# Performance work log

Hardware: AMD Instinct MI355X
Metric: run time of the kernel (lower is better)

## Reference

```python
import jax, jax.numpy as jnp
import numpy as np

# dims (see shape_source)
B, NC, DIM_IN = 4, 4095, 64      # batch, cells, invariant state dim (n-6)
D, H, L, K = 128, 4, 2, 6        # d_model, heads, layers, num_neighbors
DH = D // H                      # dim_head = 32
HR, NRBF = 16, 16                # radial hidden dim (d_model//8), rbf basis
RBF_MAX, RBF_W = 4.0, 0.25


def _ln(x, s, b):
    m = x.mean(-1, keepdims=True)
    v = x.var(-1, keepdims=True)
    return (x - m) / jnp.sqrt(v + 1e-5) * s + b


def setup_inputs() -> dict:
    key = jax.random.key(0)
    ks = jax.random.split(key, 32)
    def nrm(k, shape, scale):
        return jax.random.normal(k, shape, jnp.float32) * scale
    p = {}
    p['X'] = nrm(ks[0], (B, NC, 6 + DIM_IN), 1.0)
    p['W_embed'] = nrm(ks[1], (DIM_IN, D), DIM_IN ** -0.5)
    p['b_embed'] = jnp.zeros((D,), jnp.float32)
    p['Wq'] = nrm(ks[2], (L, D, D), D ** -0.5)
    p['Wk'] = nrm(ks[3], (L, D, D), D ** -0.5)
    p['Wv'] = nrm(ks[4], (L, D, D), D ** -0.5)
    p['Wvv'] = nrm(ks[5], (L, D, D), D ** -0.5)
    p['rw1'] = nrm(ks[6], (L, NRBF, HR), NRBF ** -0.5)
    p['rb1'] = jnp.zeros((L, HR), jnp.float32)
    p['rw2'] = nrm(ks[7], (L, HR, 2 * D), HR ** -0.5)
    p['rb2'] = jnp.zeros((L, 2 * D), jnp.float32)
    p['Wo'] = nrm(ks[8], (L, D, D), D ** -0.5)
    p['Wov'] = nrm(ks[9], (L, D, D), D ** -0.5)
    p['ff_w1'] = nrm(ks[10], (L, D, 2 * D), D ** -0.5)
    p['ff_b1'] = jnp.zeros((L, 2 * D), jnp.float32)
    p['ff_w2'] = nrm(ks[11], (L, 2 * D, D), (2 * D) ** -0.5)
    p['ff_b2'] = jnp.zeros((L, D), jnp.float32)
    p['gate_w'] = nrm(ks[12], (L, D, D), D ** -0.5)
    p['gate_b'] = jnp.zeros((L, D), jnp.float32)
    p['ln1_s'] = jnp.ones((L, D), jnp.float32)
    p['ln1_b'] = jnp.zeros((L, D), jnp.float32)
    p['ln2_s'] = jnp.ones((L, D), jnp.float32)
    p['ln2_b'] = jnp.zeros((L, D), jnp.float32)
    p['W_state'] = nrm(ks[13], (D, DIM_IN), D ** -0.5)
    p['b_state'] = jnp.zeros((DIM_IN,), jnp.float32)
    p['W_force'] = nrm(ks[14], (D, 1), D ** -0.5)
    p['b_force'] = jnp.zeros((1,), jnp.float32)
    return p


def _forward(X, W_embed, b_embed, Wq, Wk, Wv, Wvv, rw1, rb1, rw2, rb2, Wo, Wov,
             ff_w1, ff_b1, ff_w2, ff_b2, gate_w, gate_b,
             ln1_s, ln1_b, ln2_s, ln2_b, W_state, b_state, W_force, b_force):
    N = NC + 1  # one extra zero node prepended, as in the torch wrapper
    pos = jnp.concatenate([jnp.zeros((B, 1, 3), X.dtype), X[:, :, 0:3]], axis=1)       # [B,N,3]
    feats = jnp.concatenate([jnp.zeros((B, 1, DIM_IN), X.dtype), X[:, :, 6:]], axis=1)  # [B,N,dim_in]

    # k-nearest-neighbor graph (indices are non-differentiable constants)
    d2 = jnp.sum((pos[:, :, None, :] - pos[:, None, :, :]) ** 2, axis=-1)  # [B,N,N]
    d2 = d2 + jnp.eye(N, dtype=X.dtype) * 1e9                               # exclude self
    _, idx = jax.lax.top_k(-d2, K)                                           # [B,N,K]

    gat = lambda a: jax.vmap(lambda ai, ii: ai[ii])(a, idx)  # [B,N,...] -> [B,N,K,...]

    rel = gat(pos) - pos[:, :, None, :]                      # [B,N,K,3]
    dist = jnp.sqrt(jnp.sum(rel ** 2, axis=-1) + 1e-8)       # [B,N,K]
    u = rel / dist[..., None]                                # unit vectors (degree-1 SH)
    centers = jnp.linspace(0.0, RBF_MAX, NRBF).astype(X.dtype)
    rbf = jnp.exp(-((dist[..., None] - centers) / RBF_W) ** 2)  # [B,N,K,NRBF]

    x0 = feats @ W_embed + b_embed                           # type-0 (invariant) feats
    x1 = jnp.zeros((B, N, D, 3), X.dtype)                    # type-1 (vector) feats

    for l in range(L):
        h = _ln(x0, ln1_s[l], ln1_b[l])
        q = (h @ Wq[l]).reshape(B, N, H, DH)
        kj = gat(h @ Wk[l]).reshape(B, N, K, H, DH)
        vj = gat(h @ Wv[l])                                   # [B,N,K,D]
        # radial MLP on distances -> invariant edge weights
        rad = jax.nn.silu(rbf @ rw1[l] + rb1[l]) @ rw2[l] + rb2[l]  # [B,N,K,2D]
        rg, rv = rad[..., :D], rad[..., D:]
        bias = rg.reshape(B, N, K, H, DH).mean(-1)            # [B,N,K,H]
        logits = jnp.einsum('bnhd,bnkhd->bnhk', q, kj) / np.float32(np.sqrt(DH))
        logits = logits + bias.transpose(0, 1, 3, 2)
        attn = jax.nn.softmax(logits, axis=-1)                # over K neighbors
        # degree-0 messages
        m0 = (vj * jax.nn.silu(rv)).reshape(B, N, K, H, DH)
        out0 = jnp.einsum('bnhk,bnkhd->bnhd', attn, m0).reshape(B, N, D)
        x0 = x0 + out0 @ Wo[l]
        # degree-1 messages: channel-mixed neighbor vectors + radial-weighted unit dirs
        x1j = gat(x1)                                          # [B,N,K,D,3]
        m1 = jnp.einsum('bnkdc,de->bnkec', x1j, Wvv[l]) + rv[..., None] * u[:, :, :, None, :]
        m1 = m1.reshape(B, N, K, H, DH, 3)
        out1 = jnp.einsum('bnhk,bnkhdc->bnhdc', attn, m1).reshape(B, N, D, 3)
        x1 = x1 + jnp.einsum('bndc,de->bnec', out1, Wov[l])
        # feed-forward on invariants + invariant gating of vectors (equivariant)
        h2 = _ln(x0, ln2_s[l], ln2_b[l])
        x0 = x0 + jax.nn.silu(h2 @ ff_w1[l] + ff_b1[l]) @ ff_w2[l] + ff_b2[l]
        x1 = x1 * jax.nn.sigmoid(h2 @ gate_w[l] + gate_b[l])[..., None]

    y0 = x0[:, 1:]                                            # drop extra node
    y1 = jnp.swapaxes(x1[:, 1:], -1, -2)                      # [B,NC,3,D]
    state_update = y0 @ W_state + b_state                     # [B,NC,dim_in]
    forces = (y1 @ W_force + b_force)[..., 0]                 # [B,NC,3]
    forces = forces - forces.mean(axis=1, keepdims=True)      # remove net force
    return state_update, forces


def reference(X, W_embed, b_embed, Wq, Wk, Wv, Wvv, rw1, rb1, rw2, rb2, Wo, Wov,
              ff_w1, ff_b1, ff_w2, ff_b2, gate_w, gate_b,
              ln1_s, ln1_b, ln2_s, ln2_b, W_state, b_state, W_force, b_force):
    return _forward(X, W_embed, b_embed, Wq, Wk, Wv, Wvv, rw1, rb1, rw2, rb2, Wo, Wov,
                    ff_w1, ff_b1, ff_w2, ff_b2, gate_w, gate_b,
                    ln1_s, ln1_b, ln2_s, ln2_b, W_state, b_state, W_force, b_force)
```

## Files before the change

kernel.cpp:

```cpp
#include <hip/hip_runtime.h>
#include <cstdint>
#include <cstddef>

namespace {

constexpr int B_ = 4, NC_ = 4095, N_ = 4096, DIN_ = 64, D_ = 128, K_ = 6;
constexpr int XROW_ = 6 + DIN_;
constexpr int ROWS_ = B_ * N_;
constexpr int KNQ = 2;
constexpr int KCAP = 32;

typedef unsigned short u16;
typedef unsigned int u32;
typedef unsigned long long u64;
typedef __attribute__((ext_vector_type(8))) short short8;
typedef __attribute__((ext_vector_type(4))) float f32x4;

__device__ __forceinline__ float sigm(float x) { return 1.f / (1.f + expf(-x)); }
__device__ __forceinline__ float silu(float x) { return x / (1.f + expf(-x)); }
__device__ __forceinline__ u16 f2bf(float x) {
    u32 u = __float_as_uint(x);
    u += 0x7FFFu + ((u >> 16) & 1u);
    return (u16)(u >> 16);
}
__device__ __forceinline__ float bf2f(u16 x) {
    return __uint_as_float(((u32)x) << 16);
}

__device__ __forceinline__ void prep_body(const float* __restrict__ X, float4* __restrict__ pos4,
                                          u16* __restrict__ featsb, int g)
{
    if (g >= ROWS_ * 64) return;
    int c = g & 63, row = g >> 6;
    int b = row >> 12, n = row & (N_ - 1);
    const float* xr = X + (size_t)(b * NC_ + n - 1) * XROW_;
    featsb[g] = (n > 0) ? f2bf(xr[6 + c]) : (u16)0;
    if (c == 0) {
        float4 p = {0.f, 0.f, 0.f, 0.f};
        if (n > 0) { p.x = xr[0]; p.y = xr[1]; p.z = xr[2]; }
        pos4[row] = p;
    }
}

__device__ __forceinline__ void prepw_body(int l, int g,
    const float* Wq, const float* Wk, const float* Wv, const float* gw,
    const float* fw1, const float* gb_, const float* fb1, const float* Wvv,
    const float* Wov, const float* Wo_, const float* fw2, const float* rw2,
    const float* rb2, const float* W_embed, const float* rw1,
    u16* WqkvT, u16* Wc2T, u16* WvvT, u16* WovT, u16* WoT, u16* fw2T, u16* WembT,
    float* bias2, float* rwg, float* rw1T, float* rw2vT)
{
    const float* Wq_l = Wq + l * 16384;  const float* Wk_l = Wk + l * 16384;
    const float* Wv_l = Wv + l * 16384;  const float* gw_l = gw + l * 16384;
    const float* fw1_l = fw1 + l * 32768; const float* gb_l = gb_ + l * 128;
    const float* fb1_l = fb1 + l * 256;  const float* Wvv_l = Wvv + l * 16384;
    const float* Wov_l = Wov + l * 16384; const float* Wo_ll = Wo_ + l * 16384;
    const float* fw2_l = fw2 + l * 32768; const float* rw2_l = rw2 + l * 4096;
    const float* rb2_l = rb2 + l * 256;  const float* rw1_l = rw1 + l * 256;

    if (g < 49152) {
        int n = g >> 7, k = g & 127;
        const float* src = (n < 128) ? Wq_l : ((n < 256) ? Wk_l : Wv_l);
        WqkvT[l * 49152 + g] = f2bf(src[k * 128 + (n & 127)]); return;
    }
    g -= 49152;
    if (g < 49152) {
        int n = g >> 7, k = g & 127;
        Wc2T[l * 49152 + g] = f2bf((n < 128) ? gw_l[k * 128 + n] : fw1_l[k * 256 + (n - 128)]); return;
    }
    g -= 49152;
    if (g < 16384) { int n = g >> 7, k = g & 127; WvvT[l * 16384 + g] = f2bf(Wvv_l[k * 128 + n]); return; }
    g -= 16384;
    if (g < 16384) { int n = g >> 7, k = g & 127; WovT[l * 16384 + g] = f2bf(Wov_l[k * 128 + n]); return; }
    g -= 16384;
    if (g < 16384) { int n = g >> 7, k = g & 127; WoT[l * 16384 + g] = f2bf(Wo_ll[k * 128 + n]); return; }
    g -= 16384;
    if (g < 32768) { int n = g >> 8, k = g & 255; fw2T[l * 32768 + g] = f2bf(fw2_l[k * 128 + n]); return; }
    g -= 32768;
    if (g < 384) { bias2[l * 384 + g] = (g < 128) ? gb_l[g] : fb1_l[g - 128]; return; }
    g -= 384;
    if (g < 64) {
        int hh = g >> 2, h = g & 3;
        float a = 0.f;
        #pragma unroll
        for (int dh = 0; dh < 32; ++dh) a += rw2_l[hh * 256 + h * 32 + dh];
        rwg[l * 128 + g] = a * (1.f / 32.f); return;
    }
    g -= 64;
    if (g < 4) {
        float a = 0.f;
        #pragma unroll
        for (int dh = 0; dh < 32; ++dh) a += rb2_l[g * 32 + dh];
        rwg[l * 128 + 64 + g] = a * (1.f / 32.f); return;
    }
    g -= 4;
    if (g < 256) {
        int hh = g >> 4, rr = g & 15;
        rw1T[l * 256 + hh * 16 + rr] = rw1_l[rr * 16 + hh]; return;
    }
    g -= 256;
    if (g < 2048) {
        int t = g >> 4, hh = g & 15;
        rw2vT[l * 2048 + t * 16 + hh] = rw2_l[hh * 256 + 128 + t]; return;
    }
    g -= 2048;
    if (g < 8192 && l == 0) {
        int n = g >> 6, k = g & 63;
        WembT[g] = f2bf(W_embed[k * 128 + n]);
    }
}

__global__ void k_prepall(const float* __restrict__ X, float4* __restrict__ pos4,
                          u16* __restrict__ featsb,
                          const float* Wq, const float* Wk, const float* Wv, const float* gw,
                          const float* fw1, const float* gb_, const float* fb1, const float* Wvv,
                          const float* Wov, const float* Wo_, const float* fw2, const float* rw2,
                          const float* rb2, const float* W_embed, const float* rw1,
                          u16* WqkvT, u16* Wc2T, u16* WvvT, u16* WovT, u16* WoT, u16* fw2T,
                          u16* WembT, float* bias2, float* rwg, float* rw1T, float* rw2vT)
{
    int id = blockIdx.x;
    if (id < 4096) {
        prep_body(X, pos4, featsb, id * 256 + threadIdx.x);
    } else {
        int id2 = id - 4096;
        int l = id2 / 747, gx = id2 % 747;
        prepw_body(l, gx * 256 + threadIdx.x, Wq, Wk, Wv, gw, fw1, gb_, fb1, Wvv, Wov, Wo_,
                   fw2, rw2, rb2, W_embed, rw1, WqkvT, Wc2T, WvvT, WovT, WoT, fw2T, WembT,
                   bias2, rwg, rw1T, rw2vT);
    }
}

__device__ __forceinline__ u64 shflxor64(u64 v, int mask)
{
    int lo = __shfl_xor((int)(u32)(v & 0xffffffffull), mask, 64);
    int hi = __shfl_xor((int)(u32)(v >> 32), mask, 64);
    return ((u64)(u32)hi << 32) | (u32)lo;
}

__device__ __forceinline__ float kth7min(float v)
{
    const float BIG = 3.4e38f;
    float kth = BIG;
    #pragma unroll
    for (int r = 0; r < 7; ++r) {
        float m = v;
        #pragma unroll
        for (int off = 1; off < 64; off <<= 1) m = fminf(m, __shfl_xor(m, off, 64));
        kth = m;
        if (v == m) v = BIG;
    }
    return kth;
}

__device__ __forceinline__ void geom_write(const float4* __restrict__ pb, int q, int j,
                                           size_t e, float* __restrict__ uv,
                                           float* __restrict__ rbfv)
{
    float4 pj = pb[j], pn = pb[q];
    float rx = pj.x - pn.x, ry = pj.y - pn.y, rz = pj.z - pn.z;
    float dist = sqrtf(rx * rx + ry * ry + rz * rz + 1e-8f);
    float inv = 1.f / dist;
    uv[e * 3 + 0] = rx * inv; uv[e * 3 + 1] = ry * inv; uv[e * 3 + 2] = rz * inv;
    #pragma unroll
    for (int r = 0; r < 16; ++r) {
        float t = (dist - (4.0f / 15.0f) * r) * 4.0f;
        rbfv[e * 16 + r] = expf(-t * t);
    }
}

__global__ __launch_bounds__(256) void k_knn(const float4* __restrict__ pos4,
                                             int* __restrict__ idxv,
                                             float* __restrict__ uv,
                                             float* __restrict__ rbfv)
{
    __shared__ u64 sHits[4][KNQ][KCAP];
    __shared__ int sCnt[4][KNQ];
    const int w = threadIdx.x >> 6, lane = threadIdx.x & 63;
    const int wave = (blockIdx.x << 2) | w;
    const int b = wave >> 11;
    const int i0 = (wave & 2047) << 1;
    const float4* pb = pos4 + (size_t)b * N_;
    const float BIG = 3.4e38f;

    if (lane < KNQ) sCnt[w][lane] = 0;
    __syncthreads();

    float4 qv[KNQ];
    #pragma unroll
    for (int qq = 0; qq < KNQ; ++qq) qv[qq] = pb[i0 + qq];

    float dmin[KNQ];
    #pragma unroll
    for (int qq = 0; qq < KNQ; ++qq) dmin[qq] = BIG;
    #pragma unroll 4
    for (int it = 0; it < 64; ++it) {
        int j = lane + (it << 6);
        float4 p = pb[j];
        #pragma unroll
        for (int qq = 0; qq < KNQ; ++qq) {
            float dx = p.x - qv[qq].x, dy = p.y - qv[qq].y, dz = p.z - qv[qq].z;
            float dd = dx * dx + dy * dy + dz * dz;
            dmin[qq] = fminf(dmin[qq], dd);
        }
    }
    float T[KNQ];
    #pragma unroll
    for (int qq = 0; qq < KNQ; ++qq) T[qq] = kth7min(dmin[qq]) * 1.000002f;

    #pragma unroll 4
    for (int it = 0; it < 64; ++it) {
        int j = lane + (it << 6);
        float4 p = pb[j];
        #pragma unroll
        for (int qq = 0; qq < KNQ; ++qq) {
            float dx = p.x - qv[qq].x, dy = p.y - qv[qq].y, dz = p.z - qv[qq].z;
            float dd = dx * dx + dy * dy + dz * dz;
            if (dd <= T[qq] && j != i0 + qq) {
                int slot = atomicAdd(&sCnt[w][qq], 1);
                if (slot < KCAP)
                    sHits[w][qq][slot] = ((u64)__float_as_uint(dd) << 32) | (u32)j;
            }
        }
    }
    __syncthreads();

    const int g = lane >> 5, li = lane & 31;
    const int cnt = sCnt[w][g];
    const int q = i0 + g;
    u64 ent = (li < (cnt < KCAP ? cnt : KCAP)) ? sHits[w][g][li] : ~0ull;
    int myj = -1;
    #pragma unroll
    for (int k = 0; k < 6; ++k) {
        u64 m = ent;
        #pragma unroll
        for (int off = 1; off < 32; off <<= 1) {
            u64 o = shflxor64(m, off);
            if (o < m) m = o;
        }
        if (li == k) myj = (int)(u32)(m & 0xffffffffull);
        if (ent == m) ent = ~0ull;
    }
    if (cnt <= KCAP && li < 6) {
        size_t e = (size_t)(b * N_ + q) * 6 + li;
        idxv[e] = myj;
        geom_write(pb, q, myj, e, uv, rbfv);
    }

    u64 ovf = __ballot(li == 0 && cnt > KCAP);
    while (ovf) {
        int gl = __ffsll(ovf) - 1; ovf &= ovf - 1;
        int qq = gl >> 5;
        int qx = i0 + qq;
        float4 qp = pb[qx];
        float Tq = T[0];
        #pragma unroll
        for (int z = 1; z < KNQ; ++z) if (z == qq) Tq = T[z];
        float e0 = BIG, e1 = BIG, e2 = BIG, e3 = BIG, e4 = BIG, e5 = BIG;
        int j0 = 0, j1 = 0, j2 = 0, j3 = 0, j4 = 0, j5 = 0;
        for (int it = 0; it < 64; ++it) {
            int j = lane + (it << 6);
            float4 p = pb[j];
            float dx = p.x - qp.x, dy = p.y - qp.y, dz = p.z - qp.z;
            float dd = dx * dx + dy * dy + dz * dz;
            if (dd <= Tq && j != qx && dd < e5) {
                e5 = dd; j5 = j;
                float td; int tj;
                if (e5 < e4) { td = e4; e4 = e5; e5 = td; tj = j4; j4 = j5; j5 = tj; }
                if (e4 < e3) { td = e3; e3 = e4; e4 = td; tj = j3; j3 = j4; j4 = tj; }
                if (e3 < e2) { td = e2; e2 = e3; e3 = td; tj = j2; j2 = j3; j3 = tj; }
                if (e2 < e1) { td = e1; e1 = e2; e2 = td; tj = j1; j1 = j2; j2 = tj; }
                if (e1 < e0) { td = e0; e0 = e1; e1 = td; tj = j0; j0 = j1; j1 = tj; }
            }
        }
        u64 a0 = ((u64)__float_as_uint(e0) << 32) | (u32)j0;
        u64 a1 = ((u64)__float_as_uint(e1) << 32) | (u32)j1;
        u64 a2 = ((u64)__float_as_uint(e2) << 32) | (u32)j2;
        u64 a3 = ((u64)__float_as_uint(e3) << 32) | (u32)j3;
        u64 a4 = ((u64)__float_as_uint(e4) << 32) | (u32)j4;
        u64 a5 = ((u64)__float_as_uint(e5) << 32) | (u32)j5;
        int fj = -1;
        #pragma unroll
        for (int k = 0; k < 6; ++k) {
            u64 m = a0;
            #pragma unroll
            for (int off = 1; off < 64; off <<= 1) {
                u64 o = shflxor64(m, off);
                if (o < m) m = o;
            }
            if (a0 == m) { a0 = a1; a1 = a2; a2 = a3; a3 = a4; a4 = a5; a5 = ~0ull; }
            if (lane == k) fj = (int)(u32)(m & 0xffffffffull);
        }
        if (lane < 6) {
            size_t e = (size_t)(b * N_ + qx) * 6 + lane;
            idxv[e] = fj;
            geom_write(pb, qx, fj, e, uv, rbfv);
        }
    }
}

template<int KD, int BM, int EPI, bool LN, bool X1ACC>
__device__ __forceinline__ void mgemm_body(
    const u16* __restrict__ A, const u16* __restrict__ WT,
    const float* __restrict__ bias, const float* __restrict__ aux,
    float* __restrict__ C, u16* __restrict__ Cb, int ldc,
    const float* __restrict__ lns, const float* __restrict__ lnb,
    u16* __restrict__ lnout,
    int bx, int by, u16* sA, u16* sB, float* sLNraw)
{
    constexpr int MI = BM / 16;
    float (*sLN)[4][2] = (float(*)[4][2])sLNraw;
    const int tid = threadIdx.x;
    const int lane = tid & 63, wn = tid >> 6;
    const int m0 = bx * BM, n0 = by * 128;
    f32x4 acc[MI][2] = {};

    const bool aload = (BM == 64) || (tid < BM * 4);
    const int arow = tid >> 2, agk = tid & 3;
    const int c0 = tid * 2, c1 = tid * 2 + 1;
    const int brow0 = c0 >> 2, bgk0 = c0 & 3;
    const int brow1 = c1 >> 2, bgk1 = c1 & 3;

    uint4 ra = {}, rb0v, rb1v;
    if (aload) ra = *(const uint4*)&A[(size_t)(m0 + arow) * KD + agk * 8];
    rb0v = *(const uint4*)&WT[(size_t)(n0 + brow0) * KD + bgk0 * 8];
    rb1v = *(const uint4*)&WT[(size_t)(n0 + brow1) * KD + bgk1 * 8];

    #pragma unroll
    for (int k0 = 0; k0 < KD; k0 += 32) {
        if (aload) *(uint4*)&sA[arow * 40 + agk * 8] = ra;
        *(uint4*)&sB[brow0 * 40 + bgk0 * 8] = rb0v;
        *(uint4*)&sB[brow1 * 40 + bgk1 * 8] = rb1v;
        __syncthreads();
        if (k0 + 32 < KD) {
            if (aload) ra = *(const uint4*)&A[(size_t)(m0 + arow) * KD + k0 + 32 + agk * 8];
            rb0v = *(const uint4*)&WT[(size_t)(n0 + brow0) * KD + k0 + 32 + bgk0 * 8];
            rb1v = *(const uint4*)&WT[(size_t)(n0 + brow1) * KD + k0 + 32 + bgk1 * 8];
        }
        const int gk = lane >> 4, lr = lane & 15;
        short8 af[MI], bfr[2];
        #pragma unroll
        for (int i = 0; i < MI; ++i)
            af[i] = *(const short8*)&sA[(i * 16 + lr) * 40 + gk * 8];
        #pragma unroll
        for (int i = 0; i < 2; ++i)
            bfr[i] = *(const short8*)&sB[(wn * 32 + i * 16 + lr) * 40 + gk * 8];
        #pragma unroll
        for (int mi = 0; mi < MI; ++mi)
            #pragma unroll
            for (int ni = 0; ni < 2; ++ni)
                acc[mi][ni] = __builtin_amdgcn_mfma_f32_16x16x32_bf16(af[mi], bfr[ni], acc[mi][ni], 0, 0, 0);
        __syncthreads();
    }

    const int lg = lane >> 4;
    const int lc = lane & 15;
    if (LN) {
        float s1[MI][4], s2[MI][4];
        #pragma unroll
        for (int mi = 0; mi < MI; ++mi) {
            int rbase = m0 + mi * 16 + lg * 4;
            #pragma unroll
            for (int ee = 0; ee < 4; ++ee) { s1[mi][ee] = 0.f; s2[mi][ee] = 0.f; }
            #pragma unroll
            for (int ni = 0; ni < 2; ++ni) {
                int col = wn * 32 + ni * 16 + lc;
                float bc = bias ? bias[col] : 0.f;
                #pragma unroll
                for (int ee = 0; ee < 4; ++ee) {
                    float v = acc[mi][ni][ee] + bc;
                    if (EPI == 1) v += C[(size_t)(rbase + ee) * 128 + col];
                    acc[mi][ni][ee] = v;
                    s1[mi][ee] += v;
                    s2[mi][ee] += v * v;
                }
            }
        }
        #pragma unroll
        for (int mi = 0; mi < MI; ++mi)
            #pragma unroll
            for (int ee = 0; ee < 4; ++ee)
                #pragma unroll
                for (int off = 1; off < 16; off <<= 1) {
                    s1[mi][ee] += __shfl_xor(s1[mi][ee], off, 64);
                    s2[mi][ee] += __shfl_xor(s2[mi][ee], off, 64);
                }
        if (lc == 0) {
            #pragma unroll
            for (int mi = 0; mi < MI; ++mi)
                #pragma unroll
                for (int ee = 0; ee < 4; ++ee) {
                    int r = mi * 16 + lg * 4 + ee;
                    sLN[r][wn][0] = s1[mi][ee];
                    sLN[r][wn][1] = s2[mi][ee];
                }
        }
        __syncthreads();
        #pragma unroll
        for (int mi = 0; mi < MI; ++mi) {
            int rbase = m0 + mi * 16 + lg * 4;
            #pragma unroll
            for (int ee = 0; ee < 4; ++ee) {
                int r = mi * 16 + lg * 4 + ee;
                float sum = sLN[r][0][0] + sLN[r][1][0] + sLN[r][2][0] + sLN[r][3][0];
                float sq  = sLN[r][0][1] + sLN[r][1][1] + sLN[r][2][1] + sLN[r][3][1];
                float mean = sum * (1.f / 128.f);
                float var = sq * (1.f / 128.f) - mean * mean;
                float inv = 1.f / sqrtf(var + 1e-5f);
                #pragma unroll
                for (int ni = 0; ni < 2; ++ni) {
                    int col = wn * 32 + ni * 16 + lc;
                    float v = acc[mi][ni][ee];
                    size_t o = (size_t)(rbase + ee) * 128 + col;
                    C[o] = v;
                    lnout[o] = f2bf((v - mean) * inv * lns[col] + lnb[col]);
                }
            }
        }
        return;
    }

    #pragma unroll
    for (int mi = 0; mi < MI; ++mi) {
        int rbase = m0 + mi * 16 + lg * 4;
        #pragma unroll
        for (int ni = 0; ni < 2; ++ni) {
            int col = n0 + wn * 32 + ni * 16 + lc;
            if (EPI == 0) {
                float bc = bias ? bias[col] : 0.f;
                #pragma unroll
                for (int ee = 0; ee < 4; ++ee)
                    C[(size_t)(rbase + ee) * ldc + col] = acc[mi][ni][ee] + bc;
            } else if (EPI == 1) {
                float bc = bias ? bias[col] : 0.f;
                #pragma unroll
                for (int ee = 0; ee < 4; ++ee) {
                    size_t o = (size_t)(rbase + ee) * ldc + col;
                    C[o] += acc[mi][ni][ee] + bc;
                }
            } else if (EPI == 2) {
                float bc = bias[col];
                if (n0 == 0) {
                    #pragma unroll
                    for (int ee = 0; ee < 4; ++ee)
                        C[(size_t)(rbase + ee) * 128 + col] = sigm(acc[mi][ni][ee] + bc);
                } else {
                    int c2 = col - 128;
                    #pragma unroll
                    for (int ee = 0; ee < 4; ++ee)
                        Cb[(size_t)(rbase + ee) * 256 + c2] = f2bf(silu(acc[mi][ni][ee] + bc));
                }
            } else if (EPI == 4) {
                float bc = bias ? bias[col] : 0.f;
                #pragma unroll
                for (int ee = 0; ee < 4; ++ee)
                    Cb[(size_t)(rbase + ee) * ldc + col] = f2bf(acc[mi][ni][ee] + bc);
            } else {
                #pragma unroll
                for (int ee = 0; ee < 4; ++ee) {
                    int m = rbase + ee;
                    size_t o = (size_t)m * 128 + col;
                    float v = acc[mi][ni][ee];
                    if (X1ACC) v += C[o];
                    v *= aux[(size_t)(m / 3) * 128 + col];
                    C[o] = v;
                    Cb[o] = f2bf(v);
                }
            }
        }
    }
}

template<int KD, int BM, int EPI, bool LN, bool X1ACC>
__global__ __launch_bounds__(256) void k_mgemm(
    const u16* __restrict__ A, const u16* __restrict__ WT,
    const float* __restrict__ bias, const float* __restrict__ aux,
    float* __restrict__ C, u16* __restrict__ Cb, int ldc,
    const float* __restrict__ lns, const float* __restrict__ lnb,
    u16* __restrict__ lnout)
{
    __shared__ u16 sA[64 * 40];
    __shared__ u16 sB[128 * 40];
    __shared__ float sLN[64 * 4 * 2];
    mgemm_body<KD, BM, EPI, LN, X1ACC>(A, WT, bias, aux, C, Cb, ldc, lns, lnb, lnout,
                                       blockIdx.x, blockIdx.y, sA, sB, sLN);
}

template<int KD0, int BM0, int EPI0, bool LN0, bool XA0,
         int KD1, int BM1, int EPI1, bool LN1v, bool XA1>
__global__ __launch_bounds__(256) void k_mgemm_dual(
    const u16* A0, const u16* WT0, const float* b0, const float* aux0,
    float* C0, u16* Cb0, int ldc0, const float* lns0, const float* lnb0, u16* ln0,
    int nx0, int nxdiv0,
    const u16* A1, const u16* WT1, const float* b1, const float* aux1,
    float* C1, u16* Cb1, int ldc1, const float* lns1, const float* lnb1, u16* ln1)
{
    __shared__ u16 sA[64 * 40];
    __shared__ u16 sB[128 * 40];
    __shared__ float sLN[64 * 4 * 2];
    int id = blockIdx.x;
    if (id < nx0) {
        mgemm_body<KD0, BM0, EPI0, LN0, XA0>(A0, WT0, b0, aux0, C0, Cb0, ldc0, lns0, lnb0, ln0,
                                             id % nxdiv0, id / nxdiv0, sA, sB, sLN);
    } else {
        id -= nx0;
        mgemm_body<KD1, BM1, EPI1, LN1v, XA1>(A1, WT1, b1, aux1, C1, Cb1, ldc1, lns1, lnb1, ln1,
                                              id, 0, sA, sB, sLN);
    }
}

template<bool HASY1>
__global__ __launch_bounds__(256) void k_attn(
    const u16* __restrict__ qkvb, const int* __restrict__ idxv,
    const float* __restrict__ rbfv, const float* __restrict__ uv,
    const u16* __restrict__ y1b,
    const float* __restrict__ rw1T, const float* __restrict__ rb1,
    const float* __restrict__ rw2vT, const float* __restrict__ rwg,
    const float* __restrict__ rb2,
    u16* __restrict__ o0b, u16* __restrict__ o1b)
{
    const int wid = threadIdx.x >> 6, lane = threadIdx.x & 63;
    const int row = blockIdx.x * 4 + wid;
    const int b = row >> 12;
    const int ch0 = lane * 2;
    const int h = lane >> 4;

    __shared__ float sHid[4][6][16];
    __shared__ float sU[4][6][3];

    int jl = 0;
    if (lane < 6) jl = idxv[row * 6 + lane];
    int jj[6];
    #pragma unroll
    for (int k = 0; k < 6; ++k) jj[k] = __shfl(jl, k, 64);

    if (lane < 18) sU[wid][lane / 3][lane % 3] = uv[(size_t)row * 18 + lane];

    {
        int idx = lane;
        #pragma unroll
        for (int rep = 0; rep < 2; ++rep) {
            if (idx < 96) {
                int k = idx >> 4, hh = idx & 15;
                float a = rb1[hh];
                const float* rb = rbfv + (size_t)(row * 6 + k) * 16;
                const float* wr = rw1T + hh * 16;
                #pragma unroll
                for (int rr = 0; rr < 16; ++rr) a += rb[rr] * wr[rr];
                sHid[wid][k][hh] = silu(a);
            }
            idx += 64;
        }
    }
    __builtin_amdgcn_wave_barrier();
    __threadfence_block();
    __builtin_amdgcn_wave_barrier();

    u32 qp = *(const u32*)&qkvb[(size_t)row * 384 + ch0];
    float q0 = bf2f((u16)qp), q1 = bf2f((u16)(qp >> 16));

    float part[6];
    #pragma unroll
    for (int k = 0; k < 6; ++k) {
        u32 kp = *(const u32*)&qkvb[(size_t)(b * N_ + jj[k]) * 384 + 128 + ch0];
        part[k] = q0 * bf2f((u16)kp) + q1 * bf2f((u16)(kp >> 16));
    }
    #pragma unroll
    for (int off = 1; off < 16; off <<= 1)
        #pragma unroll
        for (int k = 0; k < 6; ++k)
            part[k] += __shfl_xor(part[k], off, 64);

    float lg[6];
    #pragma unroll
    for (int k = 0; k < 6; ++k) {
        float bias = rwg[64 + h];
        #pragma unroll
        for (int hh = 0; hh < 16; ++hh) bias += sHid[wid][k][hh] * rwg[hh * 4 + h];
        lg[k] = part[k] * 0.17677669529663687f + bias;
    }

    float mx = lg[0];
    #pragma unroll
    for (int k = 1; k < 6; ++k) mx = fmaxf(mx, lg[k]);
    float a[6], smv = 0.f;
    #pragma unroll
    for (int k = 0; k < 6; ++k) { a[k] = expf(lg[k] - mx); smv += a[k]; }
    float inv = 1.f / smv;
    #pragma unroll
    for (int k = 0; k < 6; ++k) a[k] *= inv;

    float rwc0[16], rwc1[16];
    {
        const float4* wp = (const float4*)(rw2vT + ch0 * 16);
        #pragma unroll
        for (int i = 0; i < 4; ++i) {
            float4 v0 = wp[i], v1 = wp[i + 4];
            rwc0[i * 4 + 0] = v0.x; rwc0[i * 4 + 1] = v0.y; rwc0[i * 4 + 2] = v0.z; rwc0[i * 4 + 3] = v0.w;
            rwc1[i * 4 + 0] = v1.x; rwc1[i * 4 + 1] = v1.y; rwc1[i * 4 + 2] = v1.z; rwc1[i * 4 + 3] = v1.w;
        }
    }
    float rb20 = rb2[128 + ch0], rb21 = rb2[128 + ch0 + 1];
    float rvk0[6], rvk1[6];
    #pragma unroll
    for (int k = 0; k < 6; ++k) {
        float a0 = rb20, a1 = rb21;
        #pragma unroll
        for (int hh = 0; hh < 16; ++hh) {
            float hv = sHid[wid][k][hh];
            a0 += hv * rwc0[hh];
            a1 += hv * rwc1[hh];
        }
        rvk0[k] = a0; rvk1[k] = a1;
    }

    float o00 = 0.f, o01 = 0.f;
    #pragma unroll
    for (int k = 0; k < 6; ++k) {
        u32 vp = *(const u32*)&qkvb[(size_t)(b * N_ + jj[k]) * 384 + 256 + ch0];
        o00 += a[k] * bf2f((u16)vp) * silu(rvk0[k]);
        o01 += a[k] * bf2f((u16)(vp >> 16)) * silu(rvk1[k]);
    }
    *(u32*)&o0b[(size_t)row * 128 + ch0] = (u32)f2bf(o00) | ((u32)f2bf(o01) << 16);

    #pragma unroll
    for (int c = 0; c < 3; ++c) {
        float s0 = 0.f, s1 = 0.f;
        #pragma unroll
        for (int k = 0; k < 6; ++k) {
            float b0 = 0.f, b1 = 0.f;
            if (HASY1) {
                u32 yp = *(const u32*)&y1b[((size_t)(b * N_ + jj[k]) * 3 + c) * 128 + ch0];
                b0 = bf2f((u16)yp); b1 = bf2f((u16)(yp >> 16));
            }
            float uk = sU[wid][k][c];
            s0 += a[k] * (b0 + rvk0[k] * uk);
            s1 += a[k] * (b1 + rvk1[k] * uk);
        }
        *(u32*)&o1b[((size_t)row * 3 + c) * 128 + ch0] = (u32)f2bf(s0) | ((u32)f2bf(s1) << 16);
    }
}

__global__ __launch_bounds__(256) void k_head(
    const float* __restrict__ x0, const float* __restrict__ W_state,
    const float* __restrict__ b_state, float* __restrict__ out,
    const float* __restrict__ x1, const float* __restrict__ W_force,
    const float* __restrict__ b_force, float* __restrict__ frc)
{
    __shared__ __align__(16) float As[32 * 132];
    __shared__ __align__(16) float Ws[32 * 68];
    const int tid = threadIdx.x;
    if (blockIdx.x < 128) {
        const int tx = tid & 15, ty = tid >> 4;
        const int m0 = blockIdx.x * 128, n0 = 0;
        float acc[8][4] = {};
        for (int k0 = 0; k0 < 128; k0 += 32) {
            __syncthreads();
            #pragma unroll
            for (int r = 0; r < 4; ++r) {
                int id = tid + r * 256;
                int row = id >> 3, kq = id & 7;
                float4 a4 = *(const float4*)&x0[(size_t)(m0 + row) * 128 + k0 + kq * 4];
                As[(kq * 4 + 0) * 132 + row] = a4.x;
                As[(kq * 4 + 1) * 132 + row] = a4.y;
                As[(kq * 4 + 2) * 132 + row] = a4.z;
                As[(kq * 4 + 3) * 132 + row] = a4.w;
            }
            #pragma unroll
            for (int r = 0; r < 2; ++r) {
                int id = tid + r * 256;
                int kr = id >> 4, cq = id & 15;
                *(float4*)&Ws[kr * 68 + cq * 4] =
                    *(const float4*)&W_state[(size_t)(k0 + kr) * 64 + n0 + cq * 4];
            }
            __syncthreads();
            #pragma unroll 8
            for (int k = 0; k < 32; ++k) {
                float4 aA = *(const float4*)&As[k * 132 + ty * 8];
                float4 aB = *(const float4*)&As[k * 132 + ty * 8 + 4];
                float4 w4 = *(const float4*)&Ws[k * 68 + tx * 4];
                float av[8] = {aA.x, aA.y, aA.z, aA.w, aB.x, aB.y, aB.z, aB.w};
                float wv[4] = {w4.x, w4.y, w4.z, w4.w};
                #pragma unroll
                for (int r = 0; r < 8; ++r)
                    #pragma unroll
                    for (int j = 0; j < 4; ++j)
                        acc[r][j] += av[r] * wv[j];
            }
        }
        float bv[4];
        #pragma unroll
        for (int j = 0; j < 4; ++j) bv[j] = b_state[n0 + tx * 4 + j];
        #pragma unroll
        for (int r = 0; r < 8; ++r) {
            int m = m0 + ty * 8 + r;
            int n = m & (N_ - 1), bb2 = m >> 12;
            if (n == 0) continue;
            float* dst = out + ((size_t)(bb2 * NC_ + n - 1)) * 64 + n0 + tx * 4;
            float4 res = {acc[r][0] + bv[0], acc[r][1] + bv[1], acc[r][2] + bv[2], acc[r][3] + bv[3]};
            *(float4*)dst = res;
        }
    } else {
        int g = (blockIdx.x - 128) * 256 + tid;
        if (g >= B_ * NC_ * 3) return;
        int c = g % 3, rr = g / 3;
        int b = rr / NC_, n = rr - b * NC_;
        const float* xr = x1 + (size_t)(b * N_ + n + 1) * 384 + c * 128;
        float a = b_force[0];
        for (int d = 0; d < 128; ++d) a += xr[d] * W_force[d];
        frc[g] = a;
    }
}

__global__ __launch_bounds__(256) void k_fsum(const float* __restrict__ frc, float* __restrict__ fsum)
{
    int b = blockIdx.x / 3, c = blockIdx.x % 3;
    __shared__ float red[256];
    float a = 0.f;
    for (int n = threadIdx.x; n < NC_; n += 256) a += frc[(b * NC_ + n) * 3 + c];
    red[threadIdx.x] = a; __syncthreads();
    for (int st = 128; st > 0; st >>= 1) { if (threadIdx.x < st) red[threadIdx.x] += red[threadIdx.x + st]; __syncthreads(); }
    if (threadIdx.x == 0) fsum[blockIdx.x] = red[0] / (float)NC_;
}

__global__ void k_force2(const float* __restrict__ frc, const float* __restrict__ fsum,
                         float* __restrict__ out)
{
    int g = blockIdx.x * 256 + threadIdx.x;
    if (g >= B_ * NC_ * 3) return;
    int c = g % 3;
    int b = g / (NC_ * 3);
    out[g] = frc[g] - fsum[b * 3 + c];
}

}

extern "C" void kernel_launch(void* const* d_in, const int* in_sizes, int n_in,
                              void* d_out, int out_size, void* d_ws, size_t ws_size,
                              hipStream_t stream)
{
    const float* X       = (const float*)d_in[0];
    const float* W_embed = (const float*)d_in[1];
    const float* b_embed = (const float*)d_in[2];
    const float* Wq      = (const float*)d_in[3];
    const float* Wk      = (const float*)d_in[4];
    const float* Wv      = (const float*)d_in[5];
    const float* Wvv     = (const float*)d_in[6];
    const float* rw1     = (const float*)d_in[7];
    const float* rb1     = (const float*)d_in[8];
    const float* rw2     = (const float*)d_in[9];
    const float* rb2     = (const float*)d_in[10];
    const float* Wo      = (const float*)d_in[11];
    const float* Wov     = (const float*)d_in[12];
    const float* ff_w1   = (const float*)d_in[13];
    const float* ff_b1   = (const float*)d_in[14];
    const float* ff_w2   = (const float*)d_in[15];
    const float* ff_b2   = (const float*)d_in[16];
    const float* gate_w  = (const float*)d_in[17];
    const float* gate_b  = (const float*)d_in[18];
    const float* ln1_s   = (const float*)d_in[19];
    const float* ln1_b   = (const float*)d_in[20];
    const float* ln2_s   = (const float*)d_in[21];
    const float* ln2_b   = (const float*)d_in[22];
    const float* W_state = (const float*)d_in[23];
    const float* b_state = (const float*)d_in[24];
    const float* W_force = (const float*)d_in[25];
    const float* b_force = (const float*)d_in[26];
    (void)in_sizes; (void)n_in; (void)out_size; (void)ws_size;

    float* out = (float*)d_out;
    float* w = (float*)d_ws;

    float4* pos4  = (float4*)w;
    int*    idxv  = (int*)(w + 65536);
    float*  uv    = w + 163840;
    float*  rbfv  = w + 458752;
    u16*    featsb= (u16*)(w + 2031616);
    float*  x0    = w + 2555904;
    u16*    hbb   = (u16*)(w + 4653056);
    u16*    qkvbb = (u16*)(w + 5701632);
    float*  gb    = w + 11993088;
    u16*    o0b   = (u16*)(w + 14090240);
    u16*    o1b   = (u16*)(w + 15138816);
    float*  x1    = w + 18284544;
    u16*    x1b   = (u16*)(w + 24576000);
    u16*    t1b   = (u16*)(w + 27721728);
    u16*    y1b   = t1b;
    u16*    WqkvT = (u16*)(w + 34013184);
    u16*    Wc2T  = (u16*)(w + 34062336);
    u16*    WvvT  = (u16*)(w + 34111488);
    u16*    WovT  = (u16*)(w + 34127872);
    u16*    WoT   = (u16*)(w + 34144256);
    u16*    fw2T  = (u16*)(w + 34160640);
    u16*    WembT = (u16*)(w + 34193408);
    float*  bias2 = w + 34197504;
    float*  rwg   = w + 34198272;
    float*  rw1T  = w + 34198528;
    float*  rw2vT = w + 34199040;
    float*  frc   = (float*)featsb;
    float*  fsum  = ((float*)featsb) + 49152;

    k_prepall<<<5590, 256, 0, stream>>>(X, pos4, featsb,
                                        Wq, Wk, Wv, gate_w, ff_w1, gate_b, ff_b1,
                                        Wvv, Wov, Wo, ff_w2, rw2, rb2, W_embed, rw1,
                                        WqkvT, Wc2T, WvvT, WovT, WoT, fw2T, WembT,
                                        bias2, rwg, rw1T, rw2vT);
    k_knn<<<ROWS_ / 8, 256, 0, stream>>>(pos4, idxv, uv, rbfv);
    k_mgemm<64, 32, 0, true, true><<<dim3(512, 1), 256, 0, stream>>>(
        featsb, WembT, b_embed, nullptr, x0, nullptr, 128, ln1_s, ln1_b, hbb);

    for (int l = 0; l < 2; ++l) {
        const float* rb1_l = rb1 + l * 16;
        const float* rb2_l = rb2 + l * 256;
        const float* fb2_l = ff_b2 + l * 128;

        if (l == 0)
            k_mgemm<128, 64, 4, false, true><<<dim3(256, 3), 256, 0, stream>>>(
                hbb, WqkvT, nullptr, nullptr, nullptr, qkvbb, 384, nullptr, nullptr, nullptr);
        else
            k_mgemm_dual<128, 64, 4, false, true, 128, 64, 4, false, true><<<1536, 256, 0, stream>>>(
                hbb, WqkvT + 49152, nullptr, nullptr, nullptr, qkvbb, 384, nullptr, nullptr, nullptr,
                768, 256,
                x1b, WvvT + 16384, nullptr, nullptr, nullptr, y1b, 128, nullptr, nullptr, nullptr);
        if (l == 0)
            k_attn<false><<<ROWS_ / 4, 256, 0, stream>>>(qkvbb, idxv, rbfv, uv, nullptr,
                rw1T + l * 256, rb1_l, rw2vT + l * 2048, rwg + l * 128, rb2_l, o0b, o1b);
        else
            k_attn<true><<<ROWS_ / 4, 256, 0, stream>>>(qkvbb, idxv, rbfv, uv, y1b,
                rw1T + l * 256, rb1_l, rw2vT + l * 2048, rwg + l * 128, rb2_l, o0b, o1b);
        k_mgemm<128, 32, 1, true, true><<<dim3(512, 1), 256, 0, stream>>>(
            o0b, WoT + l * 16384, nullptr, nullptr, x0, nullptr, 128,
            ln2_s + l * 128, ln2_b + l * 128, hbb);
        k_mgemm<128, 64, 2, false, true><<<dim3(256, 3), 256, 0, stream>>>(
            hbb, Wc2T + l * 49152, bias2 + l * 384, nullptr, gb, t1b, 128, nullptr, nullptr, nullptr);
        if (l == 0)
            k_mgemm_dual<128, 64, 3, false, false, 256, 32, 1, true, true><<<1280, 256, 0, stream>>>(
                o1b, WovT, nullptr, gb, x1, x1b, 128, nullptr, nullptr, nullptr,
                768, 768,
                t1b, fw2T, fb2_l, nullptr, x0, nullptr, 128, ln1_s + 128, ln1_b + 128, hbb);
        else
            k_mgemm_dual<128, 64, 3, false, true, 256, 32, 1, false, true><<<1280, 256, 0, stream>>>(
                o1b, WovT + 16384, nullptr, gb, x1, x1b, 128, nullptr, nullptr, nullptr,
                768, 768,
                t1b, fw2T + 32768, fb2_l, nullptr, x0, nullptr, 128, nullptr, nullptr, nullptr);
    }

    k_head<<<320, 256, 0, stream>>>(x0, W_state, b_state, out, x1, W_force, b_force, frc);
    k_fsum<<<12, 256, 0, stream>>>(frc, fsum);
    k_force2<<<(B_ * NC_ * 3 + 255) / 256, 256, 0, stream>>>(frc, fsum, out + (size_t)B_ * NC_ * DIN_);
}
```

Before: 286.0 us.

## Split KNN candidate scan across wave pairs with four queries per wave

Each wave now handles four queries over half of the candidate points, and the two waves of a pair merge their per-query thresholds through shared memory. Squared distance is computed as |p|^2+|q|^2-2p·q using a precomputed norm stored in pos4.w, and the exact difference form is recomputed only for accepted hits. The aim is more reuse of each loaded point and fewer FLOPs per pair. In exchange it adds a block barrier and a looser threshold margin, which may let in more hits and trigger the slow overflow path more often.

```diff
diff --git a/kernel.cpp b/kernel.cpp
--- a/kernel.cpp
+++ b/kernel.cpp
@@ -7,7 +7,6 @@
 constexpr int B_ = 4, NC_ = 4095, N_ = 4096, DIN_ = 64, D_ = 128, K_ = 6;
 constexpr int XROW_ = 6 + DIN_;
 constexpr int ROWS_ = B_ * N_;
-constexpr int KNQ = 2;
 constexpr int KCAP = 32;
 
 typedef unsigned short u16;
@@ -37,7 +36,7 @@
     featsb[g] = (n > 0) ? f2bf(xr[6 + c]) : (u16)0;
     if (c == 0) {
         float4 p = {0.f, 0.f, 0.f, 0.f};
-        if (n > 0) { p.x = xr[0]; p.y = xr[1]; p.z = xr[2]; }
+        if (n > 0) { p.x = xr[0]; p.y = xr[1]; p.z = xr[2]; p.w = p.x * p.x + p.y * p.y + p.z * p.z; }
         pos4[row] = p;
     }
 }
@@ -174,61 +173,75 @@
                                              float* __restrict__ uv,
                                              float* __restrict__ rbfv)
 {
-    __shared__ u64 sHits[4][KNQ][KCAP];
-    __shared__ int sCnt[4][KNQ];
+    __shared__ u64 sHits[8][KCAP];
+    __shared__ int sCnt[8];
+    __shared__ float sT[4][4];
     const int w = threadIdx.x >> 6, lane = threadIdx.x & 63;
-    const int wave = (blockIdx.x << 2) | w;
-    const int b = wave >> 11;
-    const int i0 = (wave & 2047) << 1;
+    const int pair = w >> 1, half = w & 1;
+    const int qglob0 = blockIdx.x * 8 + pair * 4;
+    const int b = qglob0 >> 12;
+    const int qwb0 = qglob0 & (N_ - 1);
     const float4* pb = pos4 + (size_t)b * N_;
+    const int jbase = half * 2048;
     const float BIG = 3.4e38f;
 
-    if (lane < KNQ) sCnt[w][lane] = 0;
+    if (threadIdx.x < 8) sCnt[threadIdx.x] = 0;
     __syncthreads();
 
-    float4 qv[KNQ];
-    #pragma unroll
-    for (int qq = 0; qq < KNQ; ++qq) qv[qq] = pb[i0 + qq];
-
-    float dmin[KNQ];
-    #pragma unroll
-    for (int qq = 0; qq < KNQ; ++qq) dmin[qq] = BIG;
+    float4 qv[4];
+    #pragma unroll
+    for (int qq = 0; qq < 4; ++qq) qv[qq] = pb[qwb0 + qq];
+
+    float dmin[4] = {BIG, BIG, BIG, BIG};
     #pragma unroll 4
-    for (int it = 0; it < 64; ++it) {
-        int j = lane + (it << 6);
+    for (int it = 0; it < 32; ++it) {
+        int j = jbase + lane + (it << 6);
         float4 p = pb[j];
         #pragma unroll
-        for (int qq = 0; qq < KNQ; ++qq) {
-            float dx = p.x - qv[qq].x, dy = p.y - qv[qq].y, dz = p.z - qv[qq].z;
-            float dd = dx * dx + dy * dy + dz * dz;
+        for (int qq = 0; qq < 4; ++qq) {
+            float dot = p.x * qv[qq].x + p.y * qv[qq].y + p.z * qv[qq].z;
+            float dd = fmaf(-2.f, dot, p.w + qv[qq].w);
             dmin[qq] = fminf(dmin[qq], dd);
         }
     }
-    float T[KNQ];
-    #pragma unroll
-    for (int qq = 0; qq < KNQ; ++qq) T[qq] = kth7min(dmin[qq]) * 1.000002f;
+    {
+        float t0 = kth7min(dmin[0]);
+        float t1 = kth7min(dmin[1]);
+        float t2 = kth7min(dmin[2]);
+        float t3 = kth7min(dmin[3]);
+        if (lane == 0) { sT[w][0] = t0; sT[w][1] = t1; sT[w][2] = t2; sT[w][3] = t3; }
+    }
+    __syncthreads();
+    float T[4];
+    #pragma unroll
+    for (int qq = 0; qq < 4; ++qq)
+        T[qq] = fminf(sT[pair * 2][qq], sT[pair * 2 + 1][qq]) * 1.001f + 1e-3f;
 
     #pragma unroll 4
-    for (int it = 0; it < 64; ++it) {
-        int j = lane + (it << 6);
+    for (int it = 0; it < 32; ++it) {
+        int j = jbase + lane + (it << 6);
         float4 p = pb[j];
         #pragma unroll
-        for (int qq = 0; qq < KNQ; ++qq) {
-            float dx = p.x - qv[qq].x, dy = p.y - qv[qq].y, dz = p.z - qv[qq].z;
-            float dd = dx * dx + dy * dy + dz * dz;
-            if (dd <= T[qq] && j != i0 + qq) {
-                int slot = atomicAdd(&sCnt[w][qq], 1);
+        for (int qq = 0; qq < 4; ++qq) {
+            float dot = p.x * qv[qq].x + p.y * qv[qq].y + p.z * qv[qq].z;
+            float dd = fmaf(-2.f, dot, p.w + qv[qq].w);
+            if (dd <= T[qq] && j != qwb0 + qq) {
+                float dx = p.x - qv[qq].x, dy = p.y - qv[qq].y, dz = p.z - qv[qq].z;
+                float de = dx * dx + dy * dy + dz * dz;
+                int slot = atomicAdd(&sCnt[pair * 4 + qq], 1);
                 if (slot < KCAP)
-                    sHits[w][qq][slot] = ((u64)__float_as_uint(dd) << 32) | (u32)j;
+                    sHits[pair * 4 + qq][slot] = ((u64)__float_as_uint(de) << 32) | (u32)j;
             }
         }
     }
     __syncthreads();
 
     const int g = lane >> 5, li = lane & 31;
-    const int cnt = sCnt[w][g];
-    const int q = i0 + g;
-    u64 ent = (li < (cnt < KCAP ? cnt : KCAP)) ? sHits[w][g][li] : ~0ull;
+    const int qb = w * 2 + g;
+    const int cnt = sCnt[qb];
+    const int qglob = blockIdx.x * 8 + qb;
+    const int qwb = qglob & (N_ - 1);
+    u64 ent = (li < (cnt < KCAP ? cnt : KCAP)) ? sHits[qb][li] : ~0ull;
     int myj = -1;
     #pragma unroll
     for (int k = 0; k < 6; ++k) {
@@ -242,20 +255,19 @@
         if (ent == m) ent = ~0ull;
     }
     if (cnt <= KCAP && li < 6) {
-        size_t e = (size_t)(b * N_ + q) * 6 + li;
+        size_t e = (size_t)qglob * 6 + li;
         idxv[e] = myj;
-        geom_write(pb, q, myj, e, uv, rbfv);
+        geom_write(pb, qwb, myj, e, uv, rbfv);
     }
 
     u64 ovf = __ballot(li == 0 && cnt > KCAP);
     while (ovf) {
         int gl = __ffsll(ovf) - 1; ovf &= ovf - 1;
-        int qq = gl >> 5;
-        int qx = i0 + qq;
+        int qbo = w * 2 + (gl >> 5);
+        int qgo = blockIdx.x * 8 + qbo;
+        int qx = qgo & (N_ - 1);
         float4 qp = pb[qx];
-        float Tq = T[0];
-        #pragma unroll
-        for (int z = 1; z < KNQ; ++z) if (z == qq) Tq = T[z];
+        float Tq = fminf(sT[(qbo >> 2) * 2][qbo & 3], sT[(qbo >> 2) * 2 + 1][qbo & 3]) * 1.001f + 1e-3f;
         float e0 = BIG, e1 = BIG, e2 = BIG, e3 = BIG, e4 = BIG, e5 = BIG;
         int j0 = 0, j1 = 0, j2 = 0, j3 = 0, j4 = 0, j5 = 0;
         for (int it = 0; it < 64; ++it) {
@@ -292,7 +304,7 @@
             if (lane == k) fj = (int)(u32)(m & 0xffffffffull);
         }
         if (lane < 6) {
-            size_t e = (size_t)(b * N_ + qx) * 6 + lane;
+            size_t e = (size_t)qgo * 6 + lane;
             idxv[e] = fj;
             geom_write(pb, qx, fj, e, uv, rbfv);
         }
```

Result: no change. 291.5 us (+1.9%).
